# Performance work log

Hardware: AMD Instinct MI355X
Metric: run time of the kernel (lower is better)

Reference implementation:

```python
import jax, jax.numpy as jnp
import numpy as np

POSE_IDS = np.array([0, 4, 8, 12, 16])
BN_EPS = 1e-5


def setup_inputs() -> dict:
    key = jax.random.key(0)
    ks = jax.random.split(key, 8)
    N, C, H, W = 64, 2048, 24, 12
    P, Cl = 5, 256
    Cm = C + P * Cl  # 3328
    return {
        "x": jax.random.normal(ks[0], (N, C, H, W), jnp.float32),
        "poses": jax.random.uniform(ks[1], (N, 17, 4), jnp.float32),
        "local_w": jax.random.normal(ks[2], (P, Cl, C), jnp.float32) * 0.02,
        "local_b": jnp.zeros((P, Cl), jnp.float32),
        "local_gamma": jnp.ones((P, Cl), jnp.float32),
        "local_beta": jnp.zeros((P, Cl), jnp.float32),
        "local_mean": jax.random.normal(ks[3], (P, Cl), jnp.float32) * 0.1,
        "local_var": jax.random.uniform(ks[4], (P, Cl), jnp.float32, 0.5, 1.5),
        "merge_w": jax.random.normal(ks[5], (C, Cm), jnp.float32) * 0.02,
        "merge_b": jnp.zeros((C,), jnp.float32),
        "merge_gamma": jnp.ones((C,), jnp.float32),
        "merge_beta": jnp.zeros((C,), jnp.float32),
        "merge_mean": jax.random.normal(ks[6], (C,), jnp.float32) * 0.1,
        "merge_var": jax.random.uniform(ks[7], (C,), jnp.float32, 0.5, 1.5),
    }


def reference(x, poses, local_w, local_b, local_gamma, local_beta, local_mean,
              local_var, merge_w, merge_b, merge_gamma, merge_beta, merge_mean,
              merge_var):
    N, C, H, W = x.shape
    kp = poses[:, jnp.asarray(POSE_IDS), :]  # [N,P,4]
    # box = [left, top, w, h]; clamp to [0, 0.75]; scale whole box by confidence
    half = jnp.full_like(kp[..., 0], 0.5)
    box = jnp.stack([kp[..., 0] - 0.25, kp[..., 1] - 0.25, half, half], axis=-1)
    box = jnp.clip(box, 0.0, 0.75) * kp[..., 2:3]
    # integer ROI bounds on the feature grid (round-half-to-even like torch)
    xs = jnp.maximum(0, jnp.round(W * box[..., 0])).astype(jnp.int32)          # [N,P]
    xe = jnp.minimum(W - 1, jnp.round(W * (box[..., 0] + box[..., 2]))).astype(jnp.int32)
    ys = jnp.maximum(0, jnp.round(H * box[..., 1])).astype(jnp.int32)
    ye = jnp.minimum(H - 1, jnp.round(H * (box[..., 1] + box[..., 3]))).astype(jnp.int32)
    rows = jnp.arange(H)
    cols = jnp.arange(W)
    mh = (rows[None, None, :] >= ys[..., None]) & (rows[None, None, :] < ye[..., None])  # [N,P,H]
    mw = (cols[None, None, :] >= xs[..., None]) & (cols[None, None, :] < xe[..., None])  # [N,P,W]
    mask = (mh[..., :, None] & mw[..., None, :]).astype(x.dtype)  # [N,P,H,W]
    # masked average pool over the ROI (single pass over x)
    sums = jnp.einsum('nchw,nphw->npc', x, mask)
    area = ((ye - ys) * (xe - xs)).astype(x.dtype)
    avg = sums / jnp.where(area > 0, area, 1.0)[..., None]  # [N,P,C], 0 for empty ROIs
    # per-part 1x1 conv + BN(eval) + ReLU -> [N,P,Cl]
    loc = jnp.einsum('npc,pkc->npk', avg, local_w) + local_b[None]
    loc = (loc - local_mean[None]) * (local_gamma[None] / jnp.sqrt(local_var[None] + BN_EPS)) + local_beta[None]
    loc = jax.nn.relu(loc)
    # global max pool -> [N,C]
    gfeat = x.max(axis=(2, 3))
    cat = jnp.concatenate([loc.reshape(N, -1), gfeat], axis=1)  # [N, P*Cl + C]
    # merge 1x1 conv + BN(eval) + ReLU
    y = cat @ merge_w.T + merge_b
    y = (y - merge_mean) * (merge_gamma / jnp.sqrt(merge_var + BN_EPS)) + merge_beta
    y = jax.nn.relu(y)
    # F.normalize(p=2, dim=1)
    norm = jnp.linalg.norm(y, axis=1, keepdims=True)
    return y / jnp.maximum(norm, 1e-12)
```

## Files before the change

kernel.cpp:

```cpp
#include <hip/hip_runtime.h>

#define N_   64
#define C_   2048
#define HW_  288
#define P_   5
#define CM_  3328
#define LOC_ 1280
#define SEGC 8
#define SEGM 13

#define PITCH  28
#define WPITCH 72

typedef __attribute__((ext_vector_type(8))) short bf16x8;
typedef __attribute__((ext_vector_type(4))) float f32x4;

__device__ __forceinline__ unsigned short f2bf(float f) {
  unsigned u = __float_as_uint(f);
  u = (u + 0x7FFFu + ((u >> 16) & 1u)) >> 16;
  return (unsigned short)u;
}
__device__ __forceinline__ unsigned pack2(float lo, float hi) {
  return (unsigned)f2bf(lo) | ((unsigned)f2bf(hi) << 16);
}

__global__ __launch_bounds__(256) void kB(const float* __restrict__ x,
    const float* __restrict__ poses,
    unsigned short* __restrict__ avgB, unsigned short* __restrict__ catB) {
  __shared__ float lds[2][256 * PITCH];
  const int t  = threadIdx.x;
  const int n  = blockIdx.x >> 3;
  const int cb = (blockIdx.x & 7) << 8;
  const int chbase = n * C_ + cb;

  unsigned MH[P_], MW[P_];
  float INV[P_];
  const float* kpn = poses + (size_t)n * 68;
#pragma unroll
  for (int p = 0; p < P_; ++p) {
    const float* kp = kpn + 16 * p;
    float px = kp[0], py = kp[1], z = kp[2];
    float bx = fminf(fmaxf(px - 0.25f, 0.f), 0.75f) * z;
    float by = fminf(fmaxf(py - 0.25f, 0.f), 0.75f) * z;
    float bw = 0.5f * z;
    float bh = 0.5f * z;
    int xs = (int)fmaxf(0.f,  rintf(12.f * bx));
    int xe = (int)fminf(11.f, rintf(12.f * (bx + bw)));
    int ys = (int)fmaxf(0.f,  rintf(24.f * by));
    int ye = (int)fminf(23.f, rintf(24.f * (by + bh)));
    MH[p] = ((1u << ye) - 1u) & ~((1u << ys) - 1u);
    MW[p] = ((1u << xe) - 1u) & ~((1u << xs) - 1u);
    int area = (ye - ys) * (xe - xs);
    INV[p] = area > 0 ? 1.f / (float)area : 1.f;
  }

  const float4* x4 = (const float4*)x;
  size_t gbase[6];
  int    loff[6];
#pragma unroll
  for (int k = 0; k < 6; ++k) {
    unsigned flat = k * 256 + t;
    unsigned cl = flat / 6u;
    unsigned j  = flat - 6u * cl;
    gbase[k] = (size_t)(chbase + cl) * 72 + j;
    loff[k]  = cl * PITCH + 4 * j;
  }

  float4 rg[6];
  auto loadRegs = [&](int ci) {
#pragma unroll
    for (int k = 0; k < 6; ++k) rg[k] = x4[gbase[k] + ci * 6];
  };
  auto writeRegs = [&](int db) {
#pragma unroll
    for (int k = 0; k < 6; ++k) *(float4*)&lds[db][loff[k]] = rg[k];
  };

  float s[P_] = {0.f, 0.f, 0.f, 0.f, 0.f};
  float mx = -3.402823466e+38f;

  loadRegs(0);
  writeRegs(0);
  __syncthreads();
  for (int ci = 0; ci < 12; ++ci) {
    if (ci + 1 < 12) loadRegs(ci + 1);
    const float* row = &lds[ci & 1][t * PITCH];
#pragma unroll
    for (int r = 0; r < 2; ++r) {
      int h = 2 * ci + r;
      float4 a = *(const float4*)(row + r * 12 + 0);
      float4 b = *(const float4*)(row + r * 12 + 4);
      float4 c = *(const float4*)(row + r * 12 + 8);
      float m1 = fmaxf(fmaxf(a.x, a.y), fmaxf(a.z, a.w));
      float m2 = fmaxf(fmaxf(b.x, b.y), fmaxf(b.z, b.w));
      float m3 = fmaxf(fmaxf(c.x, c.y), fmaxf(c.z, c.w));
      mx = fmaxf(mx, fmaxf(m1, fmaxf(m2, m3)));
#pragma unroll
      for (int p = 0; p < P_; ++p) {
        unsigned cm = ((MH[p] >> h) & 1u) ? MW[p] : 0u;
        if (cm) {
          float t0 = ((cm & 0x001u) ? a.x : 0.f) + ((cm & 0x002u) ? a.y : 0.f);
          float t1 = ((cm & 0x004u) ? a.z : 0.f) + ((cm & 0x008u) ? a.w : 0.f);
          float t2 = ((cm & 0x010u) ? b.x : 0.f) + ((cm & 0x020u) ? b.y : 0.f);
          float t3 = ((cm & 0x040u) ? b.z : 0.f) + ((cm & 0x080u) ? b.w : 0.f);
          float t4 = ((cm & 0x100u) ? c.x : 0.f) + ((cm & 0x200u) ? c.y : 0.f);
          float t5 = ((cm & 0x400u) ? c.z : 0.f) + ((cm & 0x800u) ? c.w : 0.f);
          s[p] += ((t0 + t1) + (t2 + t3)) + (t4 + t5);
        }
      }
    }
    if (ci + 1 < 12) {
      writeRegs((ci + 1) & 1);
      __syncthreads();
    }
  }

  int c = cb + t;
  catB[(size_t)n * CM_ + LOC_ + c] = f2bf(mx);
#pragma unroll
  for (int p = 0; p < P_; ++p)
    avgB[((size_t)n * 5 + p) * C_ + c] = f2bf(s[p] * INV[p]);
}

__device__ __forceinline__ void mfma_seg(const uint4* __restrict__ aRow,
                                         const float4* __restrict__ wRow,
                                         unsigned short* As, unsigned short* Ws,
                                         f32x4 acc[4]) {
  const int t  = threadIdx.x;
  const int kq = t & 3;
  const int row = t >> 2;
  const int w  = t >> 6;
  const int l  = t & 63;
  unsigned short* aw = &As[row * WPITCH + kq * 16];
  unsigned short* ww = &Ws[row * WPITCH + kq * 16];
  const int arow16 = (16 * w + (l & 15)) * WPITCH + (l >> 4) * 8;
  const int brow16 = (l & 15) * WPITCH + (l >> 4) * 8;
  for (int g = 0; g < 4; ++g) {
    uint4 a0 = aRow[g * 8 + 0], a1 = aRow[g * 8 + 1];
    float4 w0 = wRow[g * 16 + 0], w1 = wRow[g * 16 + 1],
           w2 = wRow[g * 16 + 2], w3 = wRow[g * 16 + 3];
    uint4 pw0, pw1;
    pw0.x = pack2(w0.x, w0.y); pw0.y = pack2(w0.z, w0.w);
    pw0.z = pack2(w1.x, w1.y); pw0.w = pack2(w1.z, w1.w);
    pw1.x = pack2(w2.x, w2.y); pw1.y = pack2(w2.z, w2.w);
    pw1.z = pack2(w3.x, w3.y); pw1.w = pack2(w3.z, w3.w);
    if (g) __syncthreads();
    *(uint4*)aw = a0; *(uint4*)(aw + 8) = a1;
    *(uint4*)ww = pw0; *(uint4*)(ww + 8) = pw1;
    __syncthreads();
#pragma unroll
    for (int s = 0; s < 2; ++s) {
      bf16x8 af = *(const bf16x8*)&As[arow16 + s * 32];
#pragma unroll
      for (int jm = 0; jm < 4; ++jm) {
        bf16x8 bf = *(const bf16x8*)&Ws[jm * 16 * WPITCH + brow16 + s * 32];
        acc[jm] = __builtin_amdgcn_mfma_f32_16x16x32_bf16(af, bf, acc[jm], 0, 0, 0);
      }
    }
  }
}

__global__ __launch_bounds__(256) void kC(const unsigned short* __restrict__ avgB,
                                          const float* __restrict__ local_w,
                                          float* __restrict__ locP) {
  __shared__ unsigned short As[64 * WPITCH];
  __shared__ unsigned short Ws[64 * WPITCH];
  int b  = blockIdx.x;
  int p  = b >> 5;
  int kt = (b >> 3) & 3;
  int sg = b & 7;
  const int t = threadIdx.x, row = t >> 2, kq = t & 3, w = t >> 6, l = t & 63;
  const uint4*  aRow = (const uint4*)avgB + ((size_t)row * 5 + p) * 256 + sg * 32 + kq * 2;
  const float4* wRow = (const float4*)(local_w + ((size_t)p * 256 + kt * 64 + row) * C_
                                       + sg * 256 + kq * 16);
  f32x4 acc[4] = {{0,0,0,0},{0,0,0,0},{0,0,0,0},{0,0,0,0}};
  mfma_seg(aRow, wRow, As, Ws, acc);
  float* outp = locP + (size_t)sg * (N_ * LOC_);
#pragma unroll
  for (int jm = 0; jm < 4; ++jm)
#pragma unroll
    for (int r = 0; r < 4; ++r)
      outp[(size_t)(16 * w + (l >> 4) * 4 + r) * LOC_ + p * 256 + kt * 64 + jm * 16 + (l & 15)]
        = acc[jm][r];
}

__global__ __launch_bounds__(256) void kC2(const float* __restrict__ locP,
    const float* __restrict__ lb, const float* __restrict__ lg, const float* __restrict__ lbe,
    const float* __restrict__ lm, const float* __restrict__ lv,
    unsigned short* __restrict__ catB) {
  int i = blockIdx.x * 256 + threadIdx.x;
  int n = i / LOC_;
  int q = i - n * LOC_;
  float s = 0.f;
#pragma unroll
  for (int sg = 0; sg < SEGC; ++sg) s += locP[(size_t)sg * (N_ * LOC_) + i];
  float sc = lg[q] / sqrtf(lv[q] + 1e-5f);
  float v = (s + lb[q] - lm[q]) * sc + lbe[q];
  catB[(size_t)n * CM_ + q] = f2bf(fmaxf(v, 0.f));
}

__global__ __launch_bounds__(256) void kD(const unsigned short* __restrict__ catB,
                                          const float* __restrict__ merge_w,
                                          float* __restrict__ mrgP) {
  __shared__ unsigned short As[64 * WPITCH];
  __shared__ unsigned short Ws[64 * WPITCH];
  int b  = blockIdx.x;
  int jt = b / SEGM;
  int sg = b - jt * SEGM;
  const int t = threadIdx.x, row = t >> 2, kq = t & 3, w = t >> 6, l = t & 63;
  const uint4*  aRow = (const uint4*)catB + (size_t)row * 416 + sg * 32 + kq * 2;
  const float4* wRow = (const float4*)(merge_w + (size_t)(jt * 64 + row) * CM_
                                       + sg * 256 + kq * 16);
  f32x4 acc[4] = {{0,0,0,0},{0,0,0,0},{0,0,0,0},{0,0,0,0}};
  mfma_seg(aRow, wRow, As, Ws, acc);
  float* outp = mrgP + (size_t)sg * (N_ * C_);
#pragma unroll
  for (int jm = 0; jm < 4; ++jm)
#pragma unroll
    for (int r = 0; r < 4; ++r)
      outp[(size_t)(16 * w + (l >> 4) * 4 + r) * C_ + jt * 64 + jm * 16 + (l & 15)]
        = acc[jm][r];
}

__global__ __launch_bounds__(256) void kE(const float* __restrict__ mrgP,
    const float* __restrict__ mb, const float* __restrict__ mg, const float* __restrict__ mbe,
    const float* __restrict__ mm, const float* __restrict__ mv,
    float* __restrict__ out) {
  int n = blockIdx.x, t = threadIdx.x;
  float z[8]; float ss = 0.f;
#pragma unroll
  for (int r = 0; r < 8; ++r) {
    int j = t + (r << 8);
    float y = 0.f;
#pragma unroll
    for (int sg = 0; sg < SEGM; ++sg) y += mrgP[(size_t)sg * (N_ * C_) + (size_t)n * C_ + j];
    float sc = mg[j] / sqrtf(mv[j] + 1e-5f);
    float v = (y + mb[j] - mm[j]) * sc + mbe[j];
    v = fmaxf(v, 0.f);
    z[r] = v; ss += v * v;
  }
#pragma unroll
  for (int off = 32; off; off >>= 1) ss += __shfl_xor(ss, off, 64);
  __shared__ float red[4];
  if ((t & 63) == 0) red[t >> 6] = ss;
  __syncthreads();
  float tot = red[0] + red[1] + red[2] + red[3];
  float inv = 1.f / fmaxf(sqrtf(tot), 1e-12f);
#pragma unroll
  for (int r = 0; r < 8; ++r) out[(size_t)n * C_ + t + (r << 8)] = z[r] * inv;
}

extern "C" void kernel_launch(void* const* d_in, const int* in_sizes, int n_in,
                              void* d_out, int out_size, void* d_ws, size_t ws_size,
                              hipStream_t stream) {
  const float* x          = (const float*)d_in[0];
  const float* poses      = (const float*)d_in[1];
  const float* local_w    = (const float*)d_in[2];
  const float* local_b    = (const float*)d_in[3];
  const float* local_g    = (const float*)d_in[4];
  const float* local_be   = (const float*)d_in[5];
  const float* local_m    = (const float*)d_in[6];
  const float* local_v    = (const float*)d_in[7];
  const float* merge_w    = (const float*)d_in[8];
  const float* merge_b    = (const float*)d_in[9];
  const float* merge_g    = (const float*)d_in[10];
  const float* merge_be   = (const float*)d_in[11];
  const float* merge_m    = (const float*)d_in[12];
  const float* merge_v    = (const float*)d_in[13];

  char* ws = (char*)d_ws;
  unsigned short* catB = (unsigned short*)ws;
  unsigned short* avgB = (unsigned short*)(ws + 425984);
  float* locP = (float*)(ws + 1736704);
  float* mrgP = (float*)(ws + 4358144);

  kB<<<512, 256, 0, stream>>>(x, poses, avgB, catB);
  kC<<<20 * SEGC, 256, 0, stream>>>(avgB, local_w, locP);
  kC2<<<(N_ * LOC_) / 256, 256, 0, stream>>>(locP, local_b, local_g, local_be,
                                             local_m, local_v, catB);
  kD<<<32 * SEGM, 256, 0, stream>>>(catB, merge_w, mrgP);
  kE<<<N_, 256, 0, stream>>>(mrgP, merge_b, merge_g, merge_be, merge_m, merge_v,
                             (float*)d_out);
}
```

Measured before the change: 294.4 us.

## Stream x via direct global-to-LDS loads, prefetch GEMM tiles, split final normalize

```diff
diff --git a/kernel.cpp b/kernel.cpp
--- a/kernel.cpp
+++ b/kernel.cpp
@@ -9,7 +9,6 @@
 #define SEGC 8
 #define SEGM 13
 
-#define PITCH  28
 #define WPITCH 72
 
 typedef __attribute__((ext_vector_type(8))) short bf16x8;
@@ -24,10 +23,16 @@
   return (unsigned)f2bf(lo) | ((unsigned)f2bf(hi) << 16);
 }
 
+__device__ __forceinline__ void load16_lds(const float4* g, void* l) {
+  __builtin_amdgcn_global_load_lds(
+      (const __attribute__((address_space(1))) void*)g,
+      (__attribute__((address_space(3))) void*)l, 16, 0, 0);
+}
+
 __global__ __launch_bounds__(256) void kB(const float* __restrict__ x,
     const float* __restrict__ poses,
     unsigned short* __restrict__ avgB, unsigned short* __restrict__ catB) {
-  __shared__ float lds[2][256 * PITCH];
+  __shared__ float lds[2][256 * 36];
   const int t  = threadIdx.x;
   const int n  = blockIdx.x >> 3;
   const int cb = (blockIdx.x & 7) << 8;
@@ -55,39 +60,39 @@
   }
 
   const float4* x4 = (const float4*)x;
-  size_t gbase[6];
-  int    loff[6];
-#pragma unroll
-  for (int k = 0; k < 6; ++k) {
-    unsigned flat = k * 256 + t;
-    unsigned cl = flat / 6u;
-    unsigned j  = flat - 6u * cl;
-    gbase[k] = (size_t)(chbase + cl) * 72 + j;
-    loff[k]  = cl * PITCH + 4 * j;
-  }
-
-  float4 rg[6];
-  auto loadRegs = [&](int ci) {
-#pragma unroll
-    for (int k = 0; k < 6; ++k) rg[k] = x4[gbase[k] + ci * 6];
-  };
-  auto writeRegs = [&](int db) {
-#pragma unroll
-    for (int k = 0; k < 6; ++k) *(float4*)&lds[db][loff[k]] = rg[k];
-  };
+  unsigned goff[9];
+#pragma unroll
+  for (int k = 0; k < 9; ++k) {
+    unsigned slot = k * 256u + (unsigned)t;
+    unsigned ch = slot / 9u;
+    unsigned j  = slot - 9u * ch;
+    goff[k] = (unsigned)(chbase + ch) * 72u + j;
+  }
+  const unsigned wbase = ((unsigned)t & 192u) * 16u;
 
   float s[P_] = {0.f, 0.f, 0.f, 0.f, 0.f};
   float mx = -3.402823466e+38f;
 
-  loadRegs(0);
-  writeRegs(0);
+  {
+    char* base = (char*)&lds[0][0];
+#pragma unroll
+    for (int k = 0; k < 9; ++k)
+      load16_lds(x4 + goff[k], base + (k * 4096u + wbase));
+  }
+  asm volatile("s_waitcnt vmcnt(0)" ::: "memory");
   __syncthreads();
-  for (int ci = 0; ci < 12; ++ci) {
-    if (ci + 1 < 12) loadRegs(ci + 1);
-    const float* row = &lds[ci & 1][t * PITCH];
-#pragma unroll
-    for (int r = 0; r < 2; ++r) {
-      int h = 2 * ci + r;
+
+  for (int ci = 0; ci < 8; ++ci) {
+    if (ci + 1 < 8) {
+      char* base = (char*)&lds[(ci + 1) & 1][0];
+#pragma unroll
+      for (int k = 0; k < 9; ++k)
+        load16_lds(x4 + goff[k] + (ci + 1) * 9, base + (k * 4096u + wbase));
+    }
+    const float* row = &lds[ci & 1][t * 36];
+#pragma unroll
+    for (int r = 0; r < 3; ++r) {
+      int h = 3 * ci + r;
       float4 a = *(const float4*)(row + r * 12 + 0);
       float4 b = *(const float4*)(row + r * 12 + 4);
       float4 c = *(const float4*)(row + r * 12 + 8);
@@ -109,8 +114,8 @@
         }
       }
     }
-    if (ci + 1 < 12) {
-      writeRegs((ci + 1) & 1);
+    if (ci + 1 < 8) {
+      asm volatile("s_waitcnt vmcnt(0)" ::: "memory");
       __syncthreads();
     }
   }
@@ -135,10 +140,9 @@
   unsigned short* ww = &Ws[row * WPITCH + kq * 16];
   const int arow16 = (16 * w + (l & 15)) * WPITCH + (l >> 4) * 8;
   const int brow16 = (l & 15) * WPITCH + (l >> 4) * 8;
+  uint4 a0 = aRow[0], a1 = aRow[1];
+  float4 w0 = wRow[0], w1 = wRow[1], w2 = wRow[2], w3 = wRow[3];
   for (int g = 0; g < 4; ++g) {
-    uint4 a0 = aRow[g * 8 + 0], a1 = aRow[g * 8 + 1];
-    float4 w0 = wRow[g * 16 + 0], w1 = wRow[g * 16 + 1],
-           w2 = wRow[g * 16 + 2], w3 = wRow[g * 16 + 3];
     uint4 pw0, pw1;
     pw0.x = pack2(w0.x, w0.y); pw0.y = pack2(w0.z, w0.w);
     pw0.z = pack2(w1.x, w1.y); pw0.w = pack2(w1.z, w1.w);
@@ -147,6 +151,11 @@
     if (g) __syncthreads();
     *(uint4*)aw = a0; *(uint4*)(aw + 8) = a1;
     *(uint4*)ww = pw0; *(uint4*)(ww + 8) = pw1;
+    if (g < 3) {
+      a0 = aRow[g * 8 + 8];  a1 = aRow[g * 8 + 9];
+      w0 = wRow[g * 16 + 16]; w1 = wRow[g * 16 + 17];
+      w2 = wRow[g * 16 + 18]; w3 = wRow[g * 16 + 19];
+    }
     __syncthreads();
 #pragma unroll
     for (int s = 0; s < 2; ++s) {
@@ -222,32 +231,38 @@
         = acc[jm][r];
 }
 
-__global__ __launch_bounds__(256) void kE(const float* __restrict__ mrgP,
+__global__ __launch_bounds__(256) void kE1(const float* __restrict__ mrgP,
     const float* __restrict__ mb, const float* __restrict__ mg, const float* __restrict__ mbe,
     const float* __restrict__ mm, const float* __restrict__ mv,
-    float* __restrict__ out) {
-  int n = blockIdx.x, t = threadIdx.x;
-  float z[8]; float ss = 0.f;
-#pragma unroll
-  for (int r = 0; r < 8; ++r) {
-    int j = t + (r << 8);
-    float y = 0.f;
-#pragma unroll
-    for (int sg = 0; sg < SEGM; ++sg) y += mrgP[(size_t)sg * (N_ * C_) + (size_t)n * C_ + j];
-    float sc = mg[j] / sqrtf(mv[j] + 1e-5f);
-    float v = (y + mb[j] - mm[j]) * sc + mbe[j];
-    v = fmaxf(v, 0.f);
-    z[r] = v; ss += v * v;
-  }
+    float* __restrict__ z, float* __restrict__ part) {
+  int nb = blockIdx.x;
+  int n = nb >> 3, t = threadIdx.x;
+  int j = ((nb & 7) << 8) + t;
+  float y = 0.f;
+#pragma unroll
+  for (int sg = 0; sg < SEGM; ++sg) y += mrgP[(size_t)sg * (N_ * C_) + (size_t)n * C_ + j];
+  float sc = mg[j] / sqrtf(mv[j] + 1e-5f);
+  float v = (y + mb[j] - mm[j]) * sc + mbe[j];
+  v = fmaxf(v, 0.f);
+  z[(size_t)n * C_ + j] = v;
+  float ss = v * v;
 #pragma unroll
   for (int off = 32; off; off >>= 1) ss += __shfl_xor(ss, off, 64);
   __shared__ float red[4];
   if ((t & 63) == 0) red[t >> 6] = ss;
   __syncthreads();
-  float tot = red[0] + red[1] + red[2] + red[3];
+  if (t == 0) part[nb] = (red[0] + red[1]) + (red[2] + red[3]);
+}
+
+__global__ __launch_bounds__(256) void kE2(const float* __restrict__ z,
+    const float* __restrict__ part, float* __restrict__ out) {
+  int nb = blockIdx.x;
+  int n = nb >> 3, t = threadIdx.x;
+  int j = ((nb & 7) << 8) + t;
+  const float* pp = part + n * 8;
+  float tot = ((pp[0] + pp[1]) + (pp[2] + pp[3])) + ((pp[4] + pp[5]) + (pp[6] + pp[7]));
   float inv = 1.f / fmaxf(sqrtf(tot), 1e-12f);
-#pragma unroll
-  for (int r = 0; r < 8; ++r) out[(size_t)n * C_ + t + (r << 8)] = z[r] * inv;
+  out[(size_t)n * C_ + j] = z[(size_t)n * C_ + j] * inv;
 }
 
 extern "C" void kernel_launch(void* const* d_in, const int* in_sizes, int n_in,
@@ -273,12 +288,15 @@
   unsigned short* avgB = (unsigned short*)(ws + 425984);
   float* locP = (float*)(ws + 1736704);
   float* mrgP = (float*)(ws + 4358144);
+  float* z    = (float*)(ws + 1736704);
+  float* part = (float*)(ws + 2260992);
 
   kB<<<512, 256, 0, stream>>>(x, poses, avgB, catB);
   kC<<<20 * SEGC, 256, 0, stream>>>(avgB, local_w, locP);
   kC2<<<(N_ * LOC_) / 256, 256, 0, stream>>>(locP, local_b, local_g, local_be,
                                              local_m, local_v, catB);
   kD<<<32 * SEGM, 256, 0, stream>>>(catB, merge_w, mrgP);
-  kE<<<N_, 256, 0, stream>>>(mrgP, merge_b, merge_g, merge_be, merge_m, merge_v,
-                             (float*)d_out);
-}
+  kE1<<<512, 256, 0, stream>>>(mrgP, merge_b, merge_g, merge_be, merge_m, merge_v,
+                               z, part);
+  kE2<<<512, 256, 0, stream>>>(z, part, (float*)d_out);
+}
```

Result: faster. 282.3 us (-4.1%).
